# Performance work log

Hardware: AMD Instinct MI355X
Metric: run time of the kernel (lower is better)

## Reference

```python
import jax, jax.numpy as jnp
import numpy as np
import math

H = 8
KAPPA = 20.0
STAGES = 10
BN_EPS = 1e-5


def _l2norm(x, axis):
    return x / (1e-6 + jnp.linalg.norm(x, axis=axis, keepdims=True))


def _pmms(node, query_feature, mu0):
    # node: (b,c,n)  query_feature: (b,n,c)  mu0: (1,c,k)
    b = node.shape[0]
    mu = jnp.broadcast_to(mu0, (b, mu0.shape[1], mu0.shape[2]))

    def step(mu, _):
        z = jax.nn.softmax(KAPPA * jnp.einsum('bcn,bck->bnk', node, mu), axis=2)
        z = z / (1e-6 + z.sum(axis=1, keepdims=True))
        mu = _l2norm(jnp.einsum('bcn,bnk->bck', node, z), axis=1)
        return mu, None

    mu, _ = jax.lax.scan(step, mu, None, length=STAGES)
    mu = jax.lax.stop_gradient(mu)  # torch.no_grad in EM
    P = jax.lax.stop_gradient(
        jax.nn.softmax(jnp.einsum('bnc,bck->bnk', query_feature, mu), axis=2))
    return P, mu


def _conv2d_same(x, w):
    return jax.lax.conv_general_dilated(
        x, w, (1, 1), 'SAME', dimension_numbers=('NCHW', 'OIHW', 'NCHW'))


def _node_weight(x, cw1, cb1, g, be, cw2, cb2):
    # x: (b, n, ch) with n a perfect square
    b, n, ch = x.shape
    w = int(math.isqrt(n))
    y = x.transpose(0, 2, 1).reshape(b * ch, 1, w, w)
    y = _conv2d_same(y, cw1) + cb1[None, :, None, None]
    # eval-mode BatchNorm2d (running_mean=0, running_var=1)
    y = g[None, :, None, None] * (y / jnp.sqrt(1.0 + BN_EPS)) + be[None, :, None, None]
    y = jax.nn.relu(y)
    y = _conv2d_same(y, cw2) + cb2[None, :, None, None]
    y = jax.nn.sigmoid(y)
    y = y.reshape(b, ch, n).transpose(0, 2, 1)
    return x * y


def setup_inputs() -> dict:
    key = jax.random.key(0)
    ks = jax.random.split(key, 16)
    b, n, d = 16, 1024, 256
    s = 0.02
    mu_a = _l2norm(jax.random.normal(ks[6], (1, d, 5), jnp.float32) * math.sqrt(2.0 / 5), axis=1)
    mu_b = _l2norm(jax.random.normal(ks[7], (1, d, 2), jnp.float32) * math.sqrt(2.0 / 2), axis=1)
    return {
        'query': jax.random.normal(ks[0], (b, n, d), jnp.float32),
        'key': jax.random.normal(ks[1], (b, n, d), jnp.float32),
        'value': jax.random.normal(ks[2], (b, n), jnp.float32),
        'lamda': jax.random.uniform(ks[3], (1,), jnp.float32),
        'W0': jax.random.normal(ks[4], (d, d), jnp.float32) * s,
        'b0': jnp.zeros((d,), jnp.float32),
        'W1': jax.random.normal(ks[5], (d, d), jnp.float32) * s,
        'b1': jnp.zeros((d,), jnp.float32),
        'mu_a': mu_a,
        'mu_b': mu_b,
        'nw1_w1': jax.random.normal(ks[8], (16, 1, 3, 3), jnp.float32) * 0.1,
        'nw1_b1': jnp.zeros((16,), jnp.float32),
        'nw1_g': jnp.ones((16,), jnp.float32),
        'nw1_be': jnp.zeros((16,), jnp.float32),
        'nw1_w2': jax.random.normal(ks[9], (1, 16, 3, 3), jnp.float32) * 0.1,
        'nw1_b2': jnp.zeros((1,), jnp.float32),
        'nw2_w1': jax.random.normal(ks[10], (16, 1, 3, 3), jnp.float32) * 0.1,
        'nw2_b1': jnp.zeros((16,), jnp.float32),
        'nw2_g': jnp.ones((16,), jnp.float32),
        'nw2_be': jnp.zeros((16,), jnp.float32),
        'nw2_w2': jax.random.normal(ks[11], (1, 16, 3, 3), jnp.float32) * 0.1,
        'nw2_b2': jnp.zeros((1,), jnp.float32),
    }


def reference(query, key, value, lamda, W0, b0, W1, b1, mu_a, mu_b,
              nw1_w1, nw1_b1, nw1_g, nw1_be, nw1_w2, nw1_b2,
              nw2_w1, nw2_b1, nw2_g, nw2_be, nw2_w2, nw2_b2):
    b, n, d = query.shape
    dk = d // H
    scale = 1.0 / math.sqrt(dk)
    # linear projections, split heads: (b,H,n,dk)
    q_l = (query @ W0.T + b0).reshape(b, n, H, dk).transpose(0, 2, 1, 3)
    k_l = (key @ W1.T + b1).reshape(b, n, H, dk).transpose(0, 2, 1, 3)
    v = value[:, None, :, None]  # (b,1,n,1) broadcast over heads
    # global path: value-weighted mean key, elementwise multiply-reduce, relu
    key_global = jnp.mean(k_l * v, axis=-2, keepdims=True)  # (b,H,1,dk)
    whole = jax.nn.relu(jnp.sum(q_l * key_global, axis=-1, keepdims=True) * scale)
    whole = jnp.mean(whole, axis=-3)  # (b,n,1)
    # local path: standard softmax attention with scalar values (dropout eval=identity)
    scores = jnp.einsum('bhqd,bhkd->bhqk', q_l, k_l) * scale
    p_attn = jax.nn.softmax(scores, axis=-1)
    part = jnp.einsum('bhqk,bk->bhq', p_attn, value)[..., None]  # (b,H,n,1)
    part = jnp.mean(part, axis=-3)  # (b,n,1)
    f = (1.0 - lamda) * part + lamda * whole
    # PMMs prototype clustering
    qT = query.transpose(0, 2, 1)  # (b,c,n)
    P1, m1 = _pmms(qT, query, mu_a)   # (b,n,5), (b,c,5)
    P2, _ = _pmms(m1, query, mu_b)    # (b,n,2)
    q1 = _node_weight(P1, nw1_w1, nw1_b1, nw1_g, nw1_be, nw1_w2, nw1_b2)
    q2 = _node_weight(P2, nw2_w1, nw2_b1, nw2_g, nw2_be, nw2_w2, nw2_b2)
    # tree_drop eval=identity
    return jnp.concatenate((f, q1, q2), axis=-1)  # (b,n,8)
```

## Files before the change

kernel.cpp:

```cpp
#include <hip/hip_runtime.h>
#include <hip/hip_bf16.h>
#include <math.h>

#define NN 1024
#define ND 256
#define NCH 32
#define PSTRIDE 1288

typedef __hip_bfloat16 bf;

typedef __attribute__((ext_vector_type(8))) short bf16x8;
typedef __attribute__((ext_vector_type(4))) float f32x4;

#define QL_ALPHA 0.25503486216f
#define WHOLE_LN2 0.6931471805599453f

__device__ __forceinline__ float wave_reduce_sum(float v) {
#pragma unroll
    for (int off = 32; off > 0; off >>= 1) v += __shfl_down(v, off, 64);
    return v;
}
__device__ __forceinline__ float wave_allreduce_sum(float v) {
#pragma unroll
    for (int off = 1; off < 64; off <<= 1) v += __shfl_xor(v, off, 64);
    return v;
}

__global__ void zero_k(float* __restrict__ out) {
    int i = blockIdx.x * 1024 + threadIdx.x;
    out[(size_t)i * 8] = 0.f;
}

__global__ __launch_bounds__(256) void gemm2_k(
    const float* __restrict__ Aq, const float* __restrict__ Ak,
    const float* __restrict__ W0, const float* __restrict__ b0v,
    const float* __restrict__ W1, const float* __restrict__ b1v,
    bf* __restrict__ QL, bf* __restrict__ KL)
{
    const float* A; const float* Bw; const float* bias; bf* C; float alpha;
    if (blockIdx.z == 0) { A = Aq; Bw = W0; bias = b0v; C = QL; alpha = QL_ALPHA; }
    else                 { A = Ak; Bw = W1; bias = b1v; C = KL; alpha = 1.0f; }
    __shared__ short Ahi[4 * 64 * 8],  Alo[4 * 64 * 8];
    __shared__ short Bhi[16 * 64 * 8], Blo[16 * 64 * 8];
    const int t = threadIdx.x;
    const int wave = t >> 6, lane = t & 63;
    const int m0 = blockIdx.x * 64;

    f32x4 acc[4][4];
#pragma unroll
    for (int m = 0; m < 4; m++)
#pragma unroll
        for (int n = 0; n < 4; n++)
#pragma unroll
            for (int r = 0; r < 4; r++) acc[m][n][r] = 0.f;

    for (int k0 = 0; k0 < 256; k0 += 32) {
        __syncthreads();
        {
            int fm = t >> 6, ls = t & 63;
            const float* src = A + (size_t)(m0 + fm * 16 + (ls & 15)) * 256 + k0 + ((ls >> 4) * 8);
            float4 x = *(const float4*)src;
            float4 y = *(const float4*)(src + 4);
            float v[8] = {x.x, x.y, x.z, x.w, y.x, y.y, y.z, y.w};
            short h[8], l8[8];
#pragma unroll
            for (int j = 0; j < 8; j++) {
                bf hb = __float2bfloat16(v[j]);
                float hf = __bfloat162float(hb);
                bf lb = __float2bfloat16(v[j] - hf);
                h[j] = *(short*)&hb; l8[j] = *(short*)&lb;
            }
            *(bf16x8*)&Ahi[t * 8] = *(bf16x8*)h;
            *(bf16x8*)&Alo[t * 8] = *(bf16x8*)l8;
        }
#pragma unroll
        for (int i = 0; i < 4; i++) {
            int idx = t + i * 256;
            int nf = idx >> 6, ls = idx & 63;
            const float* src = Bw + (size_t)(nf * 16 + (ls & 15)) * 256 + k0 + ((ls >> 4) * 8);
            float4 x = *(const float4*)src;
            float4 y = *(const float4*)(src + 4);
            float v[8] = {x.x, x.y, x.z, x.w, y.x, y.y, y.z, y.w};
            short h[8], l8[8];
#pragma unroll
            for (int j = 0; j < 8; j++) {
                bf hb = __float2bfloat16(v[j]);
                float hf = __bfloat162float(hb);
                bf lb = __float2bfloat16(v[j] - hf);
                h[j] = *(short*)&hb; l8[j] = *(short*)&lb;
            }
            *(bf16x8*)&Bhi[idx * 8] = *(bf16x8*)h;
            *(bf16x8*)&Blo[idx * 8] = *(bf16x8*)l8;
        }
        __syncthreads();
        bf16x8 ah[4], al[4], bh[4], bl[4];
#pragma unroll
        for (int m = 0; m < 4; m++) {
            ah[m] = *(const bf16x8*)&Ahi[(m * 64 + lane) * 8];
            al[m] = *(const bf16x8*)&Alo[(m * 64 + lane) * 8];
        }
#pragma unroll
        for (int n = 0; n < 4; n++) {
            int nf = wave * 4 + n;
            bh[n] = *(const bf16x8*)&Bhi[(nf * 64 + lane) * 8];
            bl[n] = *(const bf16x8*)&Blo[(nf * 64 + lane) * 8];
        }
#pragma unroll
        for (int m = 0; m < 4; m++)
#pragma unroll
            for (int n = 0; n < 4; n++) {
                acc[m][n] = __builtin_amdgcn_mfma_f32_16x16x32_bf16(ah[m], bh[n], acc[m][n], 0, 0, 0);
                acc[m][n] = __builtin_amdgcn_mfma_f32_16x16x32_bf16(ah[m], bl[n], acc[m][n], 0, 0, 0);
                acc[m][n] = __builtin_amdgcn_mfma_f32_16x16x32_bf16(al[m], bh[n], acc[m][n], 0, 0, 0);
            }
    }
#pragma unroll
    for (int n = 0; n < 4; n++) {
        int col = (wave * 4 + n) * 16 + (lane & 15);
        float bv = bias[col];
#pragma unroll
        for (int m = 0; m < 4; m++) {
            int row = m0 + m * 16 + (lane >> 4) * 4;
#pragma unroll
            for (int r = 0; r < 4; r++) {
                bf hv = __float2bfloat16((acc[m][n][r] + bv) * alpha);
                C[(size_t)(row + r) * 256 + col] = hv;
            }
        }
    }
}

__global__ __launch_bounds__(256) void attn4_k(
    const bf* __restrict__ QL, const bf* __restrict__ KL,
    const float* __restrict__ value, const float* __restrict__ lamda,
    float* __restrict__ out)
{
    const int bh = blockIdx.x; const int b = bh >> 3, h = bh & 7;
    const int t = threadIdx.x;
    const int wave = t >> 6, lane = t & 63;
    const int q0 = blockIdx.y * 128 + wave * 32;

    __shared__ bf Kf[128 * 32];
    __shared__ float vv[128];

    bf16x8 qf[2];
    {
        const bf* qbase = QL + ((size_t)b * NN) * ND + h * 32 + (lane >> 4) * 8;
#pragma unroll
        for (int m = 0; m < 2; m++)
            qf[m] = *(const bf16x8*)(qbase + (size_t)(q0 + m * 16 + (lane & 15)) * ND);
    }
    f32x4 lsum[2], vacc[2], wacc[2];
#pragma unroll
    for (int m = 0; m < 2; m++)
#pragma unroll
        for (int r = 0; r < 4; r++) { lsum[m][r] = 0.f; vacc[m][r] = 0.f; wacc[m][r] = 0.f; }

    const bf* kbase = KL + ((size_t)b * NN) * ND + h * 32;
    for (int kt = 0; kt < 8; kt++) {
        const int k0 = kt * 128;
        __syncthreads();
#pragma unroll
        for (int i = 0; i < 2; i++) {
            int f = t + i * 256;
            int row = ((f >> 6) << 4) + (f & 15);
            int chunk = (f >> 4) & 3;
            *(bf16x8*)&Kf[f * 8] = *(const bf16x8*)(kbase + (size_t)(k0 + row) * ND + chunk * 8);
        }
        if (t < 128) vv[t] = value[(size_t)b * NN + k0 + t];
        __syncthreads();
#pragma unroll
        for (int s = 0; s < 8; s++) {
            bf16x8 bfr = *(const bf16x8*)&Kf[(s * 64 + lane) * 8];
            float vcol = vv[s * 16 + (lane & 15)];
#pragma unroll
            for (int m = 0; m < 2; m++) {
                f32x4 acc = {0.f, 0.f, 0.f, 0.f};
                acc = __builtin_amdgcn_mfma_f32_16x16x32_bf16(qf[m], bfr, acc, 0, 0, 0);
#pragma unroll
                for (int r = 0; r < 4; r++) {
                    float sraw = acc[r];
                    float p = exp2f(sraw);
                    lsum[m][r] += p;
                    vacc[m][r] += p * vcol;
                    wacc[m][r] += sraw * vcol;
                }
            }
        }
    }
    const float lam = lamda[0];
#pragma unroll
    for (int m = 0; m < 2; m++)
#pragma unroll
        for (int r = 0; r < 4; r++) {
            float ls = lsum[m][r], va = vacc[m][r], wa = wacc[m][r];
#pragma unroll
            for (int off = 1; off < 16; off <<= 1) {
                ls += __shfl_xor(ls, off, 64);
                va += __shfl_xor(va, off, 64);
                wa += __shfl_xor(wa, off, 64);
            }
            if ((lane & 15) == 0) {
                int q = q0 + m * 16 + (lane >> 4) * 4 + r;
                float part = va / ls;
                float whole = fmaxf(wa * (WHOLE_LN2 / 1024.0f), 0.f);
                float f = ((1.f - lam) * part + lam * whole) * 0.125f;
                atomicAdd(&out[((size_t)b * NN + q) * 8], f);
            }
        }
}

__global__ __launch_bounds__(256) void mu_k(
    const float* __restrict__ pin, float* __restrict__ muG)
{
    __shared__ float red[32];
    const int b = blockIdx.x, t = threadIdx.x;
    const int wave = t >> 6, lane = t & 63;
    float mr[5] = {0,0,0,0,0};
    float cs[5] = {0,0,0,0,0};
    for (int ch = 0; ch < NCH; ch++) {
        const float* pb = pin + ((size_t)(b * NCH + ch)) * PSTRIDE;
#pragma unroll
        for (int k = 0; k < 5; k++) mr[k] += pb[k * 256 + t];
#pragma unroll
        for (int k = 0; k < 5; k++) cs[k] += pb[1280 + k];
    }
#pragma unroll
    for (int k = 0; k < 5; k++) mr[k] *= 1.0f / (1e-6f + cs[k]);
#pragma unroll
    for (int k = 0; k < 5; k++) {
        float s = wave_reduce_sum(mr[k] * mr[k]);
        if (lane == 0) red[wave * 5 + k] = s;
    }
    __syncthreads();
    if (t < 5) red[20 + t] = 1.0f / (1e-6f + sqrtf(red[t] + red[5 + t] + red[10 + t] + red[15 + t]));
    __syncthreads();
#pragma unroll
    for (int k = 0; k < 5; k++)
        muG[(size_t)b * 1280 + k * 256 + t] = mr[k] * red[20 + k];
}

__global__ __launch_bounds__(256) void zacc_k(
    const float* __restrict__ query, const float* __restrict__ mu0a,
    const float* __restrict__ muG, float* __restrict__ pout, int stage)
{
    __shared__ float muT[5 * 256];
    __shared__ float z_s[32][8];
    const int chunk = blockIdx.x, b = blockIdx.y;
    const int t = threadIdx.x;

    if (stage == 0) {
        for (int idx = t; idx < 1280; idx += 256)
            muT[idx] = mu0a[(idx & 255) * 5 + (idx >> 8)];
    } else {
        for (int idx = t; idx < 1280; idx += 256)
            muT[idx] = muG[(size_t)b * 1280 + idx];
    }
    __syncthreads();

    const int n_local = t >> 3, part = t & 7;
    {
        const float* qrow = query + ((size_t)b * NN + chunk * 32 + n_local) * ND + part * 32;
        float lg[5] = {0,0,0,0,0};
#pragma unroll
        for (int c4 = 0; c4 < 32; c4 += 4) {
            float4 qv = *(const float4*)&qrow[c4];
#pragma unroll
            for (int k = 0; k < 5; k++) {
                float4 mv = *(const float4*)&muT[k * 256 + part * 32 + c4];
                lg[k] += qv.x*mv.x + qv.y*mv.y + qv.z*mv.z + qv.w*mv.w;
            }
        }
#pragma unroll
        for (int k = 0; k < 5; k++) {
            lg[k] += __shfl_xor(lg[k], 1, 64);
            lg[k] += __shfl_xor(lg[k], 2, 64);
            lg[k] += __shfl_xor(lg[k], 4, 64);
        }
        float mx = lg[0];
#pragma unroll
        for (int k = 1; k < 5; k++) mx = fmaxf(mx, lg[k]);
        float e[5], ssum = 0.f;
#pragma unroll
        for (int k = 0; k < 5; k++) { e[k] = expf(20.0f * (lg[k] - mx)); ssum += e[k]; }
        float is = 1.0f / ssum;
        if (part == 0) {
#pragma unroll
            for (int k = 0; k < 5; k++) z_s[n_local][k] = e[k] * is;
        }
    }
    __syncthreads();

    float pa[5] = {0,0,0,0,0};
    const float* qcol = query + ((size_t)b * NN + chunk * 32) * ND + t;
#pragma unroll 4
    for (int nl = 0; nl < 32; nl++) {
        float qv = qcol[(size_t)nl * ND];
        float4 z4 = *(const float4*)&z_s[nl][0];
        float z4v = z_s[nl][4];
        pa[0] += qv * z4.x; pa[1] += qv * z4.y; pa[2] += qv * z4.z;
        pa[3] += qv * z4.w; pa[4] += qv * z4v;
    }
    float* pb = pout + ((size_t)(b * NCH + chunk)) * PSTRIDE;
#pragma unroll
    for (int k = 0; k < 5; k++) pb[k * 256 + t] = pa[k];
    if (t < 5) {
        float s = 0.f;
        for (int nl = 0; nl < 32; nl++) s += z_s[nl][t];
        pb[1280 + t] = s;
    }
}

__global__ __launch_bounds__(64) void pmms_b_k(
    const float* __restrict__ pin, const float* __restrict__ mu0b,
    float* __restrict__ m1_ws, float* __restrict__ mu2_ws)
{
    int b = blockIdx.x, lane = threadIdx.x;
    float nd[5][4];
    float cs[5] = {0,0,0,0,0};
#pragma unroll
    for (int n = 0; n < 5; n++)
#pragma unroll
        for (int j = 0; j < 4; j++) nd[n][j] = 0.f;
    for (int ch = 0; ch < NCH; ch++) {
        const float* pb = pin + ((size_t)(b * NCH + ch)) * PSTRIDE;
#pragma unroll
        for (int n = 0; n < 5; n++)
#pragma unroll
            for (int j = 0; j < 4; j++) nd[n][j] += pb[n * 256 + lane + 64 * j];
#pragma unroll
        for (int n = 0; n < 5; n++) cs[n] += pb[1280 + n];
    }
#pragma unroll
    for (int n = 0; n < 5; n++) {
        float inv = 1.0f / (1e-6f + cs[n]);
        float sq = 0.f;
#pragma unroll
        for (int j = 0; j < 4; j++) { nd[n][j] *= inv; sq += nd[n][j] * nd[n][j]; }
        float s = wave_allreduce_sum(sq);
        float nr = 1.0f / (1e-6f + sqrtf(s));
#pragma unroll
        for (int j = 0; j < 4; j++) {
            nd[n][j] *= nr;
            m1_ws[((size_t)b * 5 + n) * 256 + lane + 64 * j] = nd[n][j];
        }
    }
    float mu[2][4];
#pragma unroll
    for (int k = 0; k < 2; k++)
#pragma unroll
        for (int j = 0; j < 4; j++) mu[k][j] = mu0b[(lane + 64 * j) * 2 + k];
    for (int stage = 0; stage < 10; stage++) {
        float z[5][2];
        float colsum0 = 0.f, colsum1 = 0.f;
#pragma unroll
        for (int n = 0; n < 5; n++) {
            float l0 = 0.f, l1 = 0.f;
#pragma unroll
            for (int j = 0; j < 4; j++) { l0 += nd[n][j] * mu[0][j]; l1 += nd[n][j] * mu[1][j]; }
            l0 = wave_allreduce_sum(l0);
            l1 = wave_allreduce_sum(l1);
            float a0 = 20.0f * l0, a1 = 20.0f * l1;
            float mxv = fmaxf(a0, a1);
            float e0 = expf(a0 - mxv), e1 = expf(a1 - mxv);
            float inv = 1.0f / (e0 + e1);
            z[n][0] = e0 * inv; z[n][1] = e1 * inv;
            colsum0 += z[n][0]; colsum1 += z[n][1];
        }
        float i0 = 1.0f / (1e-6f + colsum0), i1 = 1.0f / (1e-6f + colsum1);
#pragma unroll
        for (int k = 0; k < 2; k++) {
            float iv = k ? i1 : i0;
            float sq = 0.f;
            float nm[4];
#pragma unroll
            for (int j = 0; j < 4; j++) {
                float v = 0.f;
#pragma unroll
                for (int n = 0; n < 5; n++) v += nd[n][j] * z[n][k];
                v *= iv;
                nm[j] = v; sq += v * v;
            }
            float s = wave_allreduce_sum(sq);
            float nr = 1.0f / (1e-6f + sqrtf(s));
#pragma unroll
            for (int j = 0; j < 4; j++) mu[k][j] = nm[j] * nr;
        }
    }
#pragma unroll
    for (int k = 0; k < 2; k++)
#pragma unroll
        for (int j = 0; j < 4; j++) mu2_ws[((size_t)b * 2 + k) * 256 + lane + 64 * j] = mu[k][j];
}

__global__ __launch_bounds__(256) void pmap_k(
    const float* __restrict__ query, const float* __restrict__ m1_ws,
    const float* __restrict__ mu2_ws, float* __restrict__ P1, float* __restrict__ P2)
{
    __shared__ float ms[7 * 256];
    int b = blockIdx.y;
    int t = threadIdx.x;
    int n = blockIdx.x * 256 + t;
    for (int idx = t; idx < 1280; idx += 256) ms[idx] = m1_ws[(size_t)b * 1280 + idx];
    for (int idx = t; idx < 512; idx += 256) ms[1280 + idx] = mu2_ws[(size_t)b * 512 + idx];
    __syncthreads();
    const float* qrow = query + ((size_t)b * NN + n) * ND;
    float lg[7] = {0,0,0,0,0,0,0};
    for (int c4 = 0; c4 < 256; c4 += 4) {
        float4 qv = *(const float4*)&qrow[c4];
#pragma unroll
        for (int k = 0; k < 7; k++) {
            float4 mv = *(const float4*)&ms[k * 256 + c4];
            lg[k] += qv.x*mv.x + qv.y*mv.y + qv.z*mv.z + qv.w*mv.w;
        }
    }
    float mx = lg[0];
#pragma unroll
    for (int k = 1; k < 5; k++) mx = fmaxf(mx, lg[k]);
    float e[5], ssum = 0.f;
#pragma unroll
    for (int k = 0; k < 5; k++) { e[k] = expf(lg[k] - mx); ssum += e[k]; }
    float is = 1.0f / ssum;
#pragma unroll
    for (int k = 0; k < 5; k++) P1[((size_t)b * 5 + k) * NN + n] = e[k] * is;
    float mx2 = fmaxf(lg[5], lg[6]);
    float e0 = expf(lg[5] - mx2), e1 = expf(lg[6] - mx2);
    float inv = 1.0f / (e0 + e1);
    P2[((size_t)b * 2 + 0) * NN + n] = e0 * inv;
    P2[((size_t)b * 2 + 1) * NN + n] = e1 * inv;
}

__global__ __launch_bounds__(1024) void nwconv_k(
    const float* __restrict__ P1, const float* __restrict__ P2,
    const float* __restrict__ w1a, const float* __restrict__ b1a,
    const float* __restrict__ ga,  const float* __restrict__ bea,
    const float* __restrict__ w2a, const float* __restrict__ b2a,
    const float* __restrict__ w1b, const float* __restrict__ b1b,
    const float* __restrict__ gb,  const float* __restrict__ beb,
    const float* __restrict__ w2b, const float* __restrict__ b2b,
    float* __restrict__ out)
{
    __shared__ float img[34 * 34];
    __shared__ float mid[16][34 * 34];
    __shared__ float w1s[144], w2s[144], bs[16], gs[16], bes[16], b2s[1];
    int ch = blockIdx.x, b = blockIdx.y;
    int t = threadIdx.x;
    int i = t >> 5, j = t & 31;
    const float* xsrc = (ch < 5) ? &P1[((size_t)b * 5 + ch) * NN]
                                 : &P2[((size_t)b * 2 + (ch - 5)) * NN];
    if (t < 144) { w1s[t] = (ch < 5 ? w1a : w1b)[t]; w2s[t] = (ch < 5 ? w2a : w2b)[t]; }
    if (t >= 256 && t < 272) {
        int y = t - 256;
        bs[y] = (ch < 5 ? b1a : b1b)[y];
        gs[y] = (ch < 5 ? ga : gb)[y];
        bes[y] = (ch < 5 ? bea : beb)[y];
    }
    if (t == 512) b2s[0] = (ch < 5 ? b2a : b2b)[0];
    for (int idx = t; idx < 1156; idx += 1024) img[idx] = 0.f;
    for (int idx = t; idx < 16 * 1156; idx += 1024) ((float*)mid)[idx] = 0.f;
    __syncthreads();
    float xv = xsrc[t];
    img[(i + 1) * 34 + (j + 1)] = xv;
    __syncthreads();
    float r[9];
#pragma unroll
    for (int dy = 0; dy < 3; dy++)
#pragma unroll
        for (int dx = 0; dx < 3; dx++)
            r[dy * 3 + dx] = img[(i + dy) * 34 + (j + dx)];
    const float bninv = rsqrtf(1.0f + 1e-5f);
#pragma unroll
    for (int oc = 0; oc < 16; oc++) {
        float a = 0.f;
#pragma unroll
        for (int q2 = 0; q2 < 9; q2++) a += w1s[oc * 9 + q2] * r[q2];
        a += bs[oc];
        a = gs[oc] * (a * bninv) + bes[oc];
        a = fmaxf(a, 0.f);
        mid[oc][(i + 1) * 34 + (j + 1)] = a;
    }
    __syncthreads();
    float acc2 = b2s[0];
#pragma unroll
    for (int oc = 0; oc < 16; oc++)
#pragma unroll
        for (int dy = 0; dy < 3; dy++)
#pragma unroll
            for (int dx = 0; dx < 3; dx++)
                acc2 += w2s[oc * 9 + dy * 3 + dx] * mid[oc][(i + dy) * 34 + (j + dx)];
    float sig = 1.0f / (1.0f + expf(-acc2));
    out[((size_t)(b * NN + t)) * 8 + 1 + ch] = xv * sig;
}

extern "C" void kernel_launch(void* const* d_in, const int* in_sizes, int n_in,
                              void* d_out, int out_size, void* d_ws, size_t ws_size,
                              hipStream_t stream) {
    const float* query = (const float*)d_in[0];
    const float* key   = (const float*)d_in[1];
    const float* value = (const float*)d_in[2];
    const float* lamda = (const float*)d_in[3];
    const float* W0 = (const float*)d_in[4];
    const float* b0 = (const float*)d_in[5];
    const float* W1 = (const float*)d_in[6];
    const float* b1 = (const float*)d_in[7];
    const float* mu_a = (const float*)d_in[8];
    const float* mu_b = (const float*)d_in[9];
    const float* nw1_w1 = (const float*)d_in[10];
    const float* nw1_b1 = (const float*)d_in[11];
    const float* nw1_g  = (const float*)d_in[12];
    const float* nw1_be = (const float*)d_in[13];
    const float* nw1_w2 = (const float*)d_in[14];
    const float* nw1_b2 = (const float*)d_in[15];
    const float* nw2_w1 = (const float*)d_in[16];
    const float* nw2_b1 = (const float*)d_in[17];
    const float* nw2_g  = (const float*)d_in[18];
    const float* nw2_be = (const float*)d_in[19];
    const float* nw2_w2 = (const float*)d_in[20];
    const float* nw2_b2 = (const float*)d_in[21];
    float* out = (float*)d_out;

    bf* QLb = (bf*)d_ws;
    bf* KLb = (bf*)((char*)d_ws + ((size_t)8 << 20));
    float* PA   = (float*)d_ws;
    float* PB   = PA + (size_t)16 * NCH * PSTRIDE;
    float* m1w  = PB + (size_t)16 * NCH * PSTRIDE;
    float* mu2w = m1w + (size_t)16 * 1280;
    float* P1w  = mu2w + (size_t)16 * 512;
    float* P2w  = P1w + (size_t)16 * 5 * 1024;
    float* muG  = P2w + (size_t)16 * 2 * 1024;

    zero_k<<<16, 1024, 0, stream>>>(out);
    gemm2_k<<<dim3(256, 1, 2), 256, 0, stream>>>(query, key, W0, b0, W1, b1, QLb, KLb);
    attn4_k<<<dim3(128, 8), 256, 0, stream>>>(QLb, KLb, value, lamda, out);

    zacc_k<<<dim3(NCH, 16), 256, 0, stream>>>(query, mu_a, muG, PA, 0);
    for (int s = 1; s < 10; s++) {
        const float* pin = (s & 1) ? PA : PB;
        float* pout      = (s & 1) ? PB : PA;
        mu_k<<<16, 256, 0, stream>>>(pin, muG);
        zacc_k<<<dim3(NCH, 16), 256, 0, stream>>>(query, mu_a, muG, pout, s);
    }
    pmms_b_k<<<16, 64, 0, stream>>>(PB, mu_b, m1w, mu2w);
    pmap_k<<<dim3(4, 16), 256, 0, stream>>>(query, m1w, mu2w, P1w, P2w);
    nwconv_k<<<dim3(7, 16), 1024, 0, stream>>>(P1w, P2w,
                                    nw1_w1, nw1_b1, nw1_g, nw1_be, nw1_w2, nw1_b2,
                                    nw2_w1, nw2_b1, nw2_g, nw2_be, nw2_w2, nw2_b2, out);
}
```

Before: 410.7 us.

## Precompute value-weighted key mean, widen attention tiles, fuse PMMs mu update into z-accumulation

The global 'whole' path is computed algebraically through a separate value-weighted key-sum kernel and a per-query dot product, which removes the per-score wacc accumulation from the attention inner loop. The attention kernel now handles 64 queries per wave and uses a raw v_exp_f32 via inline asm. The per-stage mu normalisation kernel is folded into a 1024-thread PMMs kernel over 8 chunks that recomputes mu from the partial sums, which halves the launches in the EM loop. This trades redundant mu reduction per block and fewer, larger blocks for fewer launches and less inner-loop work.

```diff
diff --git a/kernel.cpp b/kernel.cpp
--- a/kernel.cpp
+++ b/kernel.cpp
@@ -4,7 +4,7 @@
 
 #define NN 1024
 #define ND 256
-#define NCH 32
+#define NCH 8
 #define PSTRIDE 1288
 
 typedef __hip_bfloat16 bf;
@@ -130,31 +130,54 @@
     }
 }
 
-__global__ __launch_bounds__(256) void attn4_k(
+__global__ __launch_bounds__(256) void kg_k(
+    const bf* __restrict__ KL, const float* __restrict__ value, float* __restrict__ KG)
+{
+    const int bh = blockIdx.x, b = bh >> 3, h = bh & 7;
+    const int t = threadIdx.x;
+    const int c = t & 31, rg = t >> 5;
+    float acc = 0.f;
+    const bf* kp = KL + (size_t)b * NN * ND + h * 32 + c;
+    const float* vp = value + (size_t)b * NN;
+#pragma unroll 8
+    for (int r = rg * 128; r < rg * 128 + 128; r++)
+        acc += __bfloat162float(kp[(size_t)r * ND]) * vp[r];
+    __shared__ float kgs[8][33];
+    kgs[rg][c] = acc;
+    __syncthreads();
+    if (t < 32) {
+        float s = 0.f;
+#pragma unroll
+        for (int g = 0; g < 8; g++) s += kgs[g][t];
+        KG[(size_t)bh * 32 + t] = s;
+    }
+}
+
+__global__ __launch_bounds__(256) void attn5_k(
     const bf* __restrict__ QL, const bf* __restrict__ KL,
     const float* __restrict__ value, const float* __restrict__ lamda,
-    float* __restrict__ out)
+    const float* __restrict__ KG, float* __restrict__ out)
 {
     const int bh = blockIdx.x; const int b = bh >> 3, h = bh & 7;
     const int t = threadIdx.x;
     const int wave = t >> 6, lane = t & 63;
-    const int q0 = blockIdx.y * 128 + wave * 32;
+    const int q0 = blockIdx.y * 256 + wave * 64;
 
     __shared__ bf Kf[128 * 32];
     __shared__ float vv[128];
 
-    bf16x8 qf[2];
+    bf16x8 qf[4];
     {
         const bf* qbase = QL + ((size_t)b * NN) * ND + h * 32 + (lane >> 4) * 8;
 #pragma unroll
-        for (int m = 0; m < 2; m++)
+        for (int m = 0; m < 4; m++)
             qf[m] = *(const bf16x8*)(qbase + (size_t)(q0 + m * 16 + (lane & 15)) * ND);
     }
-    f32x4 lsum[2], vacc[2], wacc[2];
-#pragma unroll
-    for (int m = 0; m < 2; m++)
-#pragma unroll
-        for (int r = 0; r < 4; r++) { lsum[m][r] = 0.f; vacc[m][r] = 0.f; wacc[m][r] = 0.f; }
+    f32x4 lsum[4], vacc[4];
+#pragma unroll
+    for (int m = 0; m < 4; m++)
+#pragma unroll
+        for (int r = 0; r < 4; r++) { lsum[m][r] = 0.f; vacc[m][r] = 0.f; }
 
     const bf* kbase = KL + ((size_t)b * NN) * ND + h * 32;
     for (int kt = 0; kt < 8; kt++) {
@@ -174,93 +197,101 @@
             bf16x8 bfr = *(const bf16x8*)&Kf[(s * 64 + lane) * 8];
             float vcol = vv[s * 16 + (lane & 15)];
 #pragma unroll
-            for (int m = 0; m < 2; m++) {
+            for (int m = 0; m < 4; m++) {
                 f32x4 acc = {0.f, 0.f, 0.f, 0.f};
                 acc = __builtin_amdgcn_mfma_f32_16x16x32_bf16(qf[m], bfr, acc, 0, 0, 0);
 #pragma unroll
                 for (int r = 0; r < 4; r++) {
-                    float sraw = acc[r];
-                    float p = exp2f(sraw);
+                    float p;
+                    asm("v_exp_f32 %0, %1\n\ts_nop 0" : "=v"(p) : "v"(acc[r]));
                     lsum[m][r] += p;
                     vacc[m][r] += p * vcol;
-                    wacc[m][r] += sraw * vcol;
                 }
             }
         }
     }
+    float kgf[8];
+#pragma unroll
+    for (int j = 0; j < 8; j++) kgf[j] = KG[(size_t)bh * 32 + (lane >> 4) * 8 + j];
     const float lam = lamda[0];
 #pragma unroll
-    for (int m = 0; m < 2; m++)
+    for (int m = 0; m < 4; m++) {
+        float dot = 0.f;
+#pragma unroll
+        for (int j = 0; j < 8; j++) {
+            float qj = __uint_as_float(((unsigned int)(unsigned short)qf[m][j]) << 16);
+            dot += qj * kgf[j];
+        }
+        dot += __shfl_xor(dot, 16, 64);
+        dot += __shfl_xor(dot, 32, 64);
 #pragma unroll
         for (int r = 0; r < 4; r++) {
-            float ls = lsum[m][r], va = vacc[m][r], wa = wacc[m][r];
+            float ls = lsum[m][r], va = vacc[m][r];
 #pragma unroll
             for (int off = 1; off < 16; off <<= 1) {
                 ls += __shfl_xor(ls, off, 64);
                 va += __shfl_xor(va, off, 64);
-                wa += __shfl_xor(wa, off, 64);
-            }
+            }
+            float dw = __shfl(dot, (lane >> 4) * 4 + r, 64);
             if ((lane & 15) == 0) {
                 int q = q0 + m * 16 + (lane >> 4) * 4 + r;
                 float part = va / ls;
-                float whole = fmaxf(wa * (WHOLE_LN2 / 1024.0f), 0.f);
+                float whole = fmaxf(dw * (WHOLE_LN2 / 1024.0f), 0.f);
                 float f = ((1.f - lam) * part + lam * whole) * 0.125f;
                 atomicAdd(&out[((size_t)b * NN + q) * 8], f);
             }
         }
-}
-
-__global__ __launch_bounds__(256) void mu_k(
-    const float* __restrict__ pin, float* __restrict__ muG)
-{
+    }
+}
+
+__global__ __launch_bounds__(1024) void pmms8_k(
+    const float* __restrict__ query, const float* __restrict__ mu0a,
+    const float* __restrict__ pin, float* __restrict__ pout, int stage)
+{
+    __shared__ float muT[5 * 256];
+    __shared__ float z_s[128][8];
     __shared__ float red[32];
-    const int b = blockIdx.x, t = threadIdx.x;
-    const int wave = t >> 6, lane = t & 63;
-    float mr[5] = {0,0,0,0,0};
-    float cs[5] = {0,0,0,0,0};
-    for (int ch = 0; ch < NCH; ch++) {
-        const float* pb = pin + ((size_t)(b * NCH + ch)) * PSTRIDE;
-#pragma unroll
-        for (int k = 0; k < 5; k++) mr[k] += pb[k * 256 + t];
-#pragma unroll
-        for (int k = 0; k < 5; k++) cs[k] += pb[1280 + k];
-    }
-#pragma unroll
-    for (int k = 0; k < 5; k++) mr[k] *= 1.0f / (1e-6f + cs[k]);
-#pragma unroll
-    for (int k = 0; k < 5; k++) {
-        float s = wave_reduce_sum(mr[k] * mr[k]);
-        if (lane == 0) red[wave * 5 + k] = s;
-    }
-    __syncthreads();
-    if (t < 5) red[20 + t] = 1.0f / (1e-6f + sqrtf(red[t] + red[5 + t] + red[10 + t] + red[15 + t]));
-    __syncthreads();
-#pragma unroll
-    for (int k = 0; k < 5; k++)
-        muG[(size_t)b * 1280 + k * 256 + t] = mr[k] * red[20 + k];
-}
-
-__global__ __launch_bounds__(256) void zacc_k(
-    const float* __restrict__ query, const float* __restrict__ mu0a,
-    const float* __restrict__ muG, float* __restrict__ pout, int stage)
-{
-    __shared__ float muT[5 * 256];
-    __shared__ float z_s[32][8];
+    __shared__ float red2[256 * 5 * 4];
     const int chunk = blockIdx.x, b = blockIdx.y;
     const int t = threadIdx.x;
+    const int wave = t >> 6, lane = t & 63;
 
     if (stage == 0) {
-        for (int idx = t; idx < 1280; idx += 256)
+        for (int idx = t; idx < 1280; idx += 1024)
             muT[idx] = mu0a[(idx & 255) * 5 + (idx >> 8)];
+        __syncthreads();
     } else {
-        for (int idx = t; idx < 1280; idx += 256)
-            muT[idx] = muG[(size_t)b * 1280 + idx];
-    }
-    __syncthreads();
-
-    const int n_local = t >> 3, part = t & 7;
+        for (int idx = t; idx < 1280; idx += 1024) {
+            int k = idx >> 8;
+            float s = 0.f, cs = 0.f;
+#pragma unroll
+            for (int ch = 0; ch < NCH; ch++) {
+                const float* pbch = pin + ((size_t)(b * NCH + ch)) * PSTRIDE;
+                s  += pbch[idx];
+                cs += pbch[1280 + k];
+            }
+            muT[idx] = s / (1e-6f + cs);
+        }
+        __syncthreads();
+        if (t < 256) {
+#pragma unroll
+            for (int k = 0; k < 5; k++) {
+                float v = muT[k * 256 + t];
+                float s = wave_reduce_sum(v * v);
+                if (lane == 0) red[wave * 5 + k] = s;
+            }
+        }
+        __syncthreads();
+        if (t < 5) red[20 + t] = 1.0f / (1e-6f + sqrtf(red[t] + red[5 + t] + red[10 + t] + red[15 + t]));
+        __syncthreads();
+        for (int idx = t; idx < 1280; idx += 1024)
+            muT[idx] *= red[20 + (idx >> 8)];
+        __syncthreads();
+    }
+
     {
-        const float* qrow = query + ((size_t)b * NN + chunk * 32 + n_local) * ND + part * 32;
+        const int n_local = t >> 3, part = t & 7;
+        const float* qrow = query + ((size_t)b * NN + chunk * 128 + n_local) * ND + part * 32;
         float lg[5] = {0,0,0,0,0};
 #pragma unroll
         for (int c4 = 0; c4 < 32; c4 += 4) {
@@ -291,22 +322,33 @@
     }
     __syncthreads();
 
-    float pa[5] = {0,0,0,0,0};
-    const float* qcol = query + ((size_t)b * NN + chunk * 32) * ND + t;
+    {
+        const int c = t & 255, rg = t >> 8;
+        float pa[5] = {0,0,0,0,0};
+        const float* qcol = query + ((size_t)b * NN + chunk * 128 + rg * 32) * ND + c;
 #pragma unroll 4
-    for (int nl = 0; nl < 32; nl++) {
-        float qv = qcol[(size_t)nl * ND];
-        float4 z4 = *(const float4*)&z_s[nl][0];
-        float z4v = z_s[nl][4];
-        pa[0] += qv * z4.x; pa[1] += qv * z4.y; pa[2] += qv * z4.z;
-        pa[3] += qv * z4.w; pa[4] += qv * z4v;
-    }
+        for (int nl = 0; nl < 32; nl++) {
+            float qv = qcol[(size_t)nl * ND];
+            float4 z4 = *(const float4*)&z_s[rg * 32 + nl][0];
+            float z4v = z_s[rg * 32 + nl][4];
+            pa[0] += qv * z4.x; pa[1] += qv * z4.y; pa[2] += qv * z4.z;
+            pa[3] += qv * z4.w; pa[4] += qv * z4v;
+        }
+#pragma unroll
+        for (int k = 0; k < 5; k++) red2[(c * 5 + k) * 4 + rg] = pa[k];
+    }
+    __syncthreads();
+
     float* pb = pout + ((size_t)(b * NCH + chunk)) * PSTRIDE;
-#pragma unroll
-    for (int k = 0; k < 5; k++) pb[k * 256 + t] = pa[k];
+    for (int idx = t; idx < 1280; idx += 1024) {
+        int c = idx & 255, k = idx >> 8;
+        const float* r4 = &red2[(c * 5 + k) * 4];
+        pb[idx] = r4[0] + r4[1] + r4[2] + r4[3];
+    }
     if (t < 5) {
         float s = 0.f;
-        for (int nl = 0; nl < 32; nl++) s += z_s[nl][t];
+#pragma unroll 8
+        for (int nl = 0; nl < 128; nl++) s += z_s[nl][t];
         pb[1280 + t] = s;
     }
 }
@@ -527,18 +569,18 @@
     float* mu2w = m1w + (size_t)16 * 1280;
     float* P1w  = mu2w + (size_t)16 * 512;
     float* P2w  = P1w + (size_t)16 * 5 * 1024;
-    float* muG  = P2w + (size_t)16 * 2 * 1024;
+    float* KGw = (float*)((char*)d_ws + ((size_t)16 << 20));
 
     zero_k<<<16, 1024, 0, stream>>>(out);
     gemm2_k<<<dim3(256, 1, 2), 256, 0, stream>>>(query, key, W0, b0, W1, b1, QLb, KLb);
-    attn4_k<<<dim3(128, 8), 256, 0, stream>>>(QLb, KLb, value, lamda, out);
-
-    zacc_k<<<dim3(NCH, 16), 256, 0, stream>>>(query, mu_a, muG, PA, 0);
+    kg_k<<<128, 256, 0, stream>>>(KLb, value, KGw);
+    attn5_k<<<dim3(128, 4), 256, 0, stream>>>(QLb, KLb, value, lamda, KGw, out);
+
+    pmms8_k<<<dim3(NCH, 16), 1024, 0, stream>>>(query, mu_a, PA, PA, 0);
     for (int s = 1; s < 10; s++) {
         const float* pin = (s & 1) ? PA : PB;
         float* pout      = (s & 1) ? PB : PA;
-        mu_k<<<16, 256, 0, stream>>>(pin, muG);
-        zacc_k<<<dim3(NCH, 16), 256, 0, stream>>>(query, mu_a, muG, pout, s);
+        pmms8_k<<<dim3(NCH, 16), 1024, 0, stream>>>(query, mu_a, pin, pout, s);
     }
     pmms_b_k<<<16, 64, 0, stream>>>(PB, mu_b, m1w, mu2w);
     pmap_k<<<dim3(4, 16), 256, 0, stream>>>(query, m1w, mu2w, P1w, P2w);
```

Measured after the change: 357.7 us. 12.9% less time.
